# Optimization experiments

Measured on AMD Instinct MI355X. Metric: run time of the kernel, lower is better.

The kernel has to match this reference:

```python
import jax, jax.numpy as jnp
import numpy as np

# ---- Cl(4,1) geometric-product Cayley table (32 blades, metric diag(+,+,+,+,-)) ----
def _build_gp_map():
    metric = [1.0, 1.0, 1.0, 1.0, -1.0]  # e1..e4 square to +1, e5 squares to -1
    gp = np.zeros((32, 32, 32), dtype=np.float32)
    for a in range(32):          # blade a as a bitmask over 5 generators
        for b in range(32):
            # sign from reordering generators into canonical order
            swaps = 0
            t = a >> 1
            while t:
                swaps += bin(t & b).count('1')
                t >>= 1
            sign = -1.0 if (swaps & 1) else 1.0
            # sign from contracted (repeated) generators via the metric
            common = a & b
            for i in range(5):
                if common & (1 << i):
                    sign *= metric[i]
            gp[a, b, a ^ b] = sign  # e_a * e_b = sign * e_{a xor b}
    return gp

GP_MAP = _build_gp_map()  # [32, 32, 32], highly sparse (one nonzero per (a,b))
EPS = 1e-6

B, S, IN, OUT = 2, 1024, 256, 256

def setup_inputs() -> dict:
    key = jax.random.key(0)
    k1, k2 = jax.random.split(key)
    x = jax.random.normal(k1, (B, S, IN, 32), dtype=jnp.float32)
    std = 1.0 / float(np.sqrt(IN * 32))  # grade-aware Xavier scale from reset_parameters
    weight = jax.random.normal(k2, (OUT, IN, 32), dtype=jnp.float32) * std
    return {"x": x, "weight": weight}

def normalize_cl41(mv):
    # normalize each multivector by its coefficient magnitude over the 32 lanes
    norm = jnp.sqrt(jnp.sum(mv * mv, axis=-1, keepdims=True) + EPS)
    return mv / norm

def reference(x, weight):
    gp = jnp.asarray(GP_MAP, dtype=x.dtype)
    # W_op[o,i,l,k] = sum_j weight[o,i,j] * gp[j,l,k]
    W_op = jnp.einsum('oij,jlk->oilk', weight, gp)
    # out[b,s,o,k] = sum_{i,l} x[b,s,i,l] * W_op[o,i,l,k]
    out = jnp.einsum('bsil,oilk->bsok', x, W_op)
    return normalize_cl41(out)
```

## Files before the change

kernel.cpp:

```cpp
#include <hip/hip_runtime.h>
#include <hip/hip_bf16.h>
#include <stdint.h>

typedef _Float16 f16;
typedef __attribute__((ext_vector_type(8))) _Float16 f16x8;
typedef __attribute__((ext_vector_type(4))) float f32x4;

#define M_DIM 2048
#define K_FULL 8192
#define M2 8192
#define K2 2048
#define N2 2048
#define BM 256
#define BN 256
#define BK 64
#define NT (K2 / BK)
#define PSTR 260

struct CMat { int re[4][4]; int im[4][4]; };

constexpr CMat cmul(const CMat& A, const CMat& B) {
  CMat C{};
  for (int r = 0; r < 4; ++r)
    for (int c = 0; c < 4; ++c) {
      int re = 0, im = 0;
      for (int t = 0; t < 4; ++t) {
        re += A.re[r][t] * B.re[t][c] - A.im[r][t] * B.im[t][c];
        im += A.re[r][t] * B.im[t][c] + A.im[r][t] * B.re[t][c];
      }
      C.re[r][c] = re; C.im[r][c] = im;
    }
  return C;
}

constexpr int gp_sign_ct(int a, int b) {
  int sw = 0;
  for (int t = a >> 1; t; t >>= 1) {
    int x = t & b;
    while (x) { sw += x & 1; x >>= 1; }
  }
  int s = (sw & 1) ? -1 : 1;
  if ((a & b) & 16) s = -s;
  return s;
}

struct Tables {
  int8_t f_idx[32][4]; int8_t f_sgn[32][4];
  int8_t g_idx[32][4]; int8_t g_sgn[32][4];
  bool ok;
};

constexpr Tables make_tables() {
  CMat G[5] = {
    { {{0,0,0,1},{0,0,1,0},{0,1,0,0},{1,0,0,0}},
      {{0,0,0,0},{0,0,0,0},{0,0,0,0},{0,0,0,0}} },
    { {{0,0,0,0},{0,0,0,0},{0,0,0,0},{0,0,0,0}},
      {{0,0,0,-1},{0,0,1,0},{0,-1,0,0},{1,0,0,0}} },
    { {{0,0,1,0},{0,0,0,-1},{1,0,0,0},{0,-1,0,0}},
      {{0,0,0,0},{0,0,0,0},{0,0,0,0},{0,0,0,0}} },
    { {{0,0,0,0},{0,0,0,0},{0,0,0,0},{0,0,0,0}},
      {{0,0,-1,0},{0,0,0,-1},{1,0,0,0},{0,1,0,0}} },
    { {{0,0,0,0},{0,0,0,0},{0,0,0,0},{0,0,0,0}},
      {{1,0,0,0},{0,1,0,0},{0,0,-1,0},{0,0,0,-1}} } };
  CMat ID{ {{1,0,0,0},{0,1,0,0},{0,0,1,0},{0,0,0,1}},
           {{0,0,0,0},{0,0,0,0},{0,0,0,0},{0,0,0,0}} };
  CMat U[32] = {};
  for (int A = 0; A < 32; ++A) {
    CMat u = ID;
    for (int b = 0; b < 5; ++b) if (A & (1 << b)) u = cmul(u, G[b]);
    U[A] = u;
  }
  bool ok = true;
  for (int a = 0; a < 32; ++a)
    for (int b = 0; b < 32; ++b) {
      CMat P = cmul(U[a], U[b]);
      int s = gp_sign_ct(a, b);
      const CMat& T = U[a ^ b];
      for (int r = 0; r < 4; ++r)
        for (int c = 0; c < 4; ++c)
          if (P.re[r][c] != s * T.re[r][c] || P.im[r][c] != s * T.im[r][c]) ok = false;
    }
  Tables t{};
  int cnt[32] = {};
  for (int A = 0; A < 32; ++A) {
    int n = 0;
    for (int r = 0; r < 4; ++r)
      for (int c = 0; c < 4; ++c) {
        int vr = U[A].re[r][c], vi = U[A].im[r][c];
        if (vr) {
          int s = (r * 4 + c) * 2;
          if (n < 4 && cnt[s] < 4) {
            t.g_idx[A][n] = (int8_t)s; t.g_sgn[A][n] = (int8_t)vr;
            t.f_idx[s][cnt[s]] = (int8_t)A; t.f_sgn[s][cnt[s]] = (int8_t)vr;
            cnt[s]++;
          } else ok = false;
          n++;
        }
        if (vi) {
          int s = (r * 4 + c) * 2 + 1;
          if (n < 4 && cnt[s] < 4) {
            t.g_idx[A][n] = (int8_t)s; t.g_sgn[A][n] = (int8_t)vi;
            t.f_idx[s][cnt[s]] = (int8_t)A; t.f_sgn[s][cnt[s]] = (int8_t)vi;
            cnt[s]++;
          } else ok = false;
          n++;
        }
      }
    if (n != 4) ok = false;
  }
  for (int s = 0; s < 32; ++s) if (cnt[s] != 4) ok = false;
  t.ok = ok;
  return t;
}

constexpr Tables HT = make_tables();
static_assert(HT.ok, "Cl(4,1) -> M(4,C) homomorphism check FAILED");
static_assert((NT & 1) == 0, "buffer parity requires even tile count");

__device__ __forceinline__ void async16(const f16* g, f16* l) {
  __builtin_amdgcn_global_load_lds(
      (const __attribute__((address_space(1))) uint32_t*)g,
      (__attribute__((address_space(3))) uint32_t*)l,
      16, 0, 0);
}

__device__ __forceinline__ float gp_sign_rt(int a, int b) {
  int sw = 0;
  for (int t = a >> 1; t; t >>= 1) sw += __popc(t & b);
  float s = (sw & 1) ? -1.0f : 1.0f;
  if ((a & b) & 16) s = -s;
  return s;
}

#define FENCE() asm volatile("" ::: "memory")
#define BARRIER() do { FENCE(); __builtin_amdgcn_s_barrier(); FENCE(); } while (0)
#define WAIT_VM(N) asm volatile("s_waitcnt vmcnt(" #N ")" ::: "memory")

__global__ __launch_bounds__(256) void fwd_kernel(const float* __restrict__ x,
                                                  const float* __restrict__ w,
                                                  f16* __restrict__ Ag,
                                                  f16* __restrict__ Bt) {
  __shared__ float xs[256 * 33];
  const int b = blockIdx.x, t = threadIdx.x;
  const bool isx = (b < M_DIM);
  const float* src0 = isx ? (x + (size_t)b * 8192)
                          : (w + (size_t)(b - M_DIM) * 8192);
  const float4* src = (const float4*)src0;
#pragma unroll
  for (int c = t; c < 2048; c += 256) {
    float4 v = src[c];
    float* d = xs + (c >> 3) * 33 + ((c & 7) << 2);
    d[0] = v.x; d[1] = v.y; d[2] = v.z; d[3] = v.w;
  }
  __syncthreads();
  const float* xv = xs + t * 33;
  float sv[32];
#pragma unroll
  for (int s = 0; s < 32; ++s)
    sv[s] = (float)HT.f_sgn[s][0] * xv[HT.f_idx[s][0]]
          + (float)HT.f_sgn[s][1] * xv[HT.f_idx[s][1]]
          + (float)HT.f_sgn[s][2] * xv[HT.f_idx[s][2]]
          + (float)HT.f_sgn[s][3] * xv[HT.f_idx[s][3]];
  if (isx) {
#pragma unroll
    for (int c = 0; c < 4; ++c) {
      f16x8 h;
#pragma unroll
      for (int e = 0; e < 8; ++e) {
        int tt = e >> 1, p = e & 1;
        h[e] = (f16)sv[tt * 8 + c * 2 + p];
      }
      *(f16x8*)(Ag + ((size_t)(b * 4 + c)) * K2 + t * 8) = h;
    }
  } else {
    const int o = b - M_DIM;
#pragma unroll
    for (int r = 0; r < 4; ++r)
#pragma unroll
      for (int q = 0; q < 2; ++q) {
        f16x8 h;
#pragma unroll
        for (int e = 0; e < 8; ++e) {
          int tt = e >> 1, p = e & 1;
          float re = sv[(r * 4 + tt) * 2], im = sv[(r * 4 + tt) * 2 + 1];
          float v = (q == 0) ? (p == 0 ? re : -im) : (p == 0 ? im : re);
          h[e] = (f16)v;
        }
        *(f16x8*)(Bt + ((size_t)(o * 8 + r * 2 + q)) * K2 + t * 8) = h;
      }
  }
}

__global__ __launch_bounds__(512, 2) void gemm_fused_kernel(const f16* __restrict__ A,
                                                            const f16* __restrict__ Bw,
                                                            float* __restrict__ out) {
  __shared__ __align__(16) char smem[131072];
  const int t = threadIdx.x;
  const int w = t >> 6, lane = t & 63;
  const int wr = w >> 2, wc = w & 3;
  const int g = lane >> 4, lc = lane & 15;

  const int bid = blockIdx.x;
  const int swzb = (bid & 7) * 32 + (bid >> 3);
  const int by = swzb >> 3, bx = swzb & 7;
  const int m0 = by * BM, n0 = bx * BN;

  const int srow = lane >> 3;
  const int schk = (lane & 7) ^ srow;
  const f16* ga0 = A  + (size_t)(m0 + w * 8 + srow) * K2 + schk * 8;
  const f16* gb0 = Bw + (size_t)(n0 + w * 8 + srow) * K2 + schk * 8;
  const int lw = w << 10;

  const int cks0 = (g ^ (lc & 7)) << 4;
  const int cks1 = ((4 | g) ^ (lc & 7)) << 4;
  const int arow = (wr << 14) + (lc << 7);
  const int brow = 32768 + (wc << 13) + (lc << 7);

  f32x4 acc[8][4];
#pragma unroll
  for (int i = 0; i < 8; ++i)
#pragma unroll
    for (int j = 0; j < 4; ++j) {
      acc[i][j][0] = 0.f; acc[i][j][1] = 0.f; acc[i][j][2] = 0.f; acc[i][j][3] = 0.f;
    }

  f16x8 avA[4][2], avB[4][2], bvA[2][2], bvB[2][2];

#define STG_A(NBO, KK, JB) async16(ga0 + (KK) + (JB) * 131072, \
                                   (f16*)(smem + (NBO) + (JB) * 8192 + lw))
#define STG_B(NBO, KK, JB) async16(gb0 + (KK) + (JB) * 131072, \
                                   (f16*)(smem + (NBO) + 32768 + (JB) * 8192 + lw))

  STG_A(0, 0, 0); STG_A(0, 0, 1); STG_A(0, 0, 2); STG_A(0, 0, 3);
  STG_B(0, 0, 0); STG_B(0, 0, 1); STG_B(0, 0, 2); STG_B(0, 0, 3);
  WAIT_VM(0);
  BARRIER();

#pragma unroll 2
  for (int u = 0; u < NT; ++u) {
    const int bo = (u & 1) << 16;
    const int nbo = bo ^ 65536;
    const int kn = (u + 1) * BK;
    const char* ab = smem + bo + arow;
    const char* bb = smem + bo + brow;
    const bool stg = (u + 1 < NT);

#pragma unroll
    for (int i = 0; i < 4; ++i) avA[i][0] = *(const f16x8*)(ab + i * 2048 + cks0);
#pragma unroll
    for (int j = 0; j < 2; ++j) bvA[j][0] = *(const f16x8*)(bb + j * 2048 + cks0);
#pragma unroll
    for (int i = 0; i < 4; ++i) avA[i][1] = *(const f16x8*)(ab + i * 2048 + cks1);
#pragma unroll
    for (int j = 0; j < 2; ++j) bvA[j][1] = *(const f16x8*)(bb + j * 2048 + cks1);

    if (stg) {
      STG_A(nbo, kn, 0); STG_A(nbo, kn, 1); STG_A(nbo, kn, 2); STG_A(nbo, kn, 3);
      STG_B(nbo, kn, 0); STG_B(nbo, kn, 1); STG_B(nbo, kn, 2); STG_B(nbo, kn, 3);
    }

    __builtin_amdgcn_s_setprio(1);
#pragma unroll
    for (int k2 = 0; k2 < 2; ++k2)
#pragma unroll
      for (int i = 0; i < 4; ++i)
#pragma unroll
        for (int j = 0; j < 2; ++j)
          acc[i][j] = __builtin_amdgcn_mfma_f32_16x16x32_f16(avA[i][k2], bvA[j][k2],
                                                             acc[i][j], 0, 0, 0);
    __builtin_amdgcn_s_setprio(0);

#pragma unroll
    for (int j = 0; j < 2; ++j) {
      bvB[j][0] = *(const f16x8*)(bb + (2 + j) * 2048 + cks0);
      bvB[j][1] = *(const f16x8*)(bb + (2 + j) * 2048 + cks1);
    }
#pragma unroll
    for (int i = 0; i < 4; ++i) {
      avB[i][0] = *(const f16x8*)(ab + (4 + i) * 2048 + cks0);
      avB[i][1] = *(const f16x8*)(ab + (4 + i) * 2048 + cks1);
    }

    __builtin_amdgcn_s_setprio(1);
#pragma unroll
    for (int k2 = 0; k2 < 2; ++k2)
#pragma unroll
      for (int i = 0; i < 4; ++i)
#pragma unroll
        for (int j = 0; j < 2; ++j)
          acc[i][2 + j] = __builtin_amdgcn_mfma_f32_16x16x32_f16(avA[i][k2], bvB[j][k2],
                                                                 acc[i][2 + j], 0, 0, 0);
    __builtin_amdgcn_s_setprio(0);

    __builtin_amdgcn_s_setprio(1);
#pragma unroll
    for (int k2 = 0; k2 < 2; ++k2)
#pragma unroll
      for (int i = 0; i < 4; ++i)
#pragma unroll
        for (int j = 0; j < 2; ++j)
          acc[4 + i][j] = __builtin_amdgcn_mfma_f32_16x16x32_f16(avB[i][k2], bvA[j][k2],
                                                                 acc[4 + i][j], 0, 0, 0);
    __builtin_amdgcn_s_setprio(0);

    __builtin_amdgcn_s_setprio(1);
#pragma unroll
    for (int k2 = 0; k2 < 2; ++k2)
#pragma unroll
      for (int i = 0; i < 4; ++i)
#pragma unroll
        for (int j = 0; j < 2; ++j)
          acc[4 + i][2 + j] = __builtin_amdgcn_mfma_f32_16x16x32_f16(avB[i][k2], bvB[j][k2],
                                                                     acc[4 + i][2 + j], 0, 0, 0);
    __builtin_amdgcn_s_setprio(0);

    if (stg) {
      WAIT_VM(0);
      BARRIER();
    }
  }

#undef STG_B
#undef STG_A

  float* ps = (float*)smem;
  __syncthreads();
#pragma unroll
  for (int qq = 0; qq < 4; ++qq) {
    if (qq) __syncthreads();
    if (wr == (qq >> 1)) {
      const int tb = (qq & 1) << 2;
#pragma unroll
      for (int tmi = 0; tmi < 4; ++tmi) {
        const int rowl = tmi * 16 + g * 4;
#pragma unroll
        for (int tn = 0; tn < 4; ++tn) {
          const int col = wc * 64 + tn * 16 + lc;
#pragma unroll
          for (int r = 0; r < 4; ++r)
            ps[(rowl + r) * PSTR + col] = acc[tb + tmi][tn][r];
        }
      }
    }
    __syncthreads();

    const int mh = t >> 5, oh = t & 31;
    float yv[4][8];
#pragma unroll
    for (int c = 0; c < 4; ++c) {
      const float* row = ps + (mh * 4 + c) * PSTR + oh * 8;
      *(float4*)&yv[c][0] = *(const float4*)row;
      *(float4*)&yv[c][4] = *(const float4*)(row + 4);
    }
    float ss = 0.f;
#pragma unroll
    for (int c = 0; c < 4; ++c)
#pragma unroll
      for (int j = 0; j < 8; ++j) ss += yv[c][j] * yv[c][j];
    float inv = rsqrtf(0.25f * ss + 1e-6f);

    float ov[32];
#pragma unroll
    for (int k = 0; k < 32; ++k) {
      float v = 0.f;
#pragma unroll
      for (int j = 0; j < 4; ++j) {
        int s = HT.g_idx[k][j];
        int cell = s >> 1;
        int rr = cell >> 2, cc = cell & 3, pp = s & 1;
        float sgn = (float)HT.g_sgn[k][j];
        v += sgn * yv[cc][rr * 2 + pp];
      }
      ov[k] = v * 0.25f * inv;
    }
    int m = by * 64 + qq * 16 + mh;
    int o = bx * 32 + oh;
    float* op = out + (size_t)m * 8192 + o * 32;
#pragma unroll
    for (int qv = 0; qv < 8; ++qv)
      *(float4*)(op + qv * 4) = make_float4(ov[qv * 4], ov[qv * 4 + 1],
                                            ov[qv * 4 + 2], ov[qv * 4 + 3]);
  }
}

__global__ __launch_bounds__(256) void naive_vl_kernel(const float* __restrict__ x,
                                                       const float* __restrict__ w,
                                                       float* __restrict__ out) {
  __shared__ float xs[8192];
  __shared__ float sgt[1024];
  int m = blockIdx.x, o0 = blockIdx.y << 3;
  int t = threadIdx.x;
  for (int i = t; i < 1024; i += 256) {
    int kk = i >> 5, ll = i & 31;
    sgt[i] = gp_sign_rt(kk ^ ll, ll);
  }
  const float4* xr = (const float4*)(x + (size_t)m * K_FULL);
  float4* xs4 = (float4*)xs;
  for (int i = t; i < 2048; i += 256) xs4[i] = xr[i];
  __syncthreads();
  int k = t & 31, ol = t >> 5;
  int o = o0 + ol;
  const float* wrow = w + (size_t)o * K_FULL;
  float acc = 0.f;
  for (int l = 0; l < 32; ++l) {
    float s = sgt[(k << 5) + l];
    const float* wp = wrow + (k ^ l);
    const float* xp = xs + l;
    float part = 0.f;
#pragma unroll 8
    for (int i = 0; i < 256; ++i) part += xp[i << 5] * wp[i << 5];
    acc += part * s;
  }
  float ss = acc * acc;
  for (int msk = 1; msk < 32; msk <<= 1) ss += __shfl_xor(ss, msk, 32);
  out[((size_t)m * 256 + o) * 32 + k] = acc * rsqrtf(ss + 1e-6f);
}

extern "C" void kernel_launch(void* const* d_in, const int* in_sizes, int n_in,
                              void* d_out, int out_size, void* d_ws, size_t ws_size,
                              hipStream_t stream) {
  const float* x = (const float*)d_in[0];
  const float* w = (const float*)d_in[1];
  float* out = (float*)d_out;

  size_t agE = (size_t)M2 * K2;
  size_t btE = (size_t)N2 * K2;
  size_t need = (agE + btE) * sizeof(f16);

  if (ws_size >= need) {
    f16* Ag = (f16*)d_ws;
    f16* Bt = Ag + agE;
    fwd_kernel<<<dim3(M_DIM + 256), dim3(256), 0, stream>>>(x, w, Ag, Bt);
    gemm_fused_kernel<<<dim3((M2 / BM) * (N2 / BN)), dim3(512), 0, stream>>>(Ag, Bt, out);
  } else {
    naive_vl_kernel<<<dim3(M_DIM, 32), dim3(256), 0, stream>>>(x, w, out);
  }
}
```

Baseline: 191.3 us.

## Use 1024-thread GEMM blocks with smaller per-wave tiles; load fwd inputs via registers

The GEMM kernel moves from 512 to 1024 threads per block. Each of the 16 waves now computes a 64x64 output tile with a 4x4 accumulator array instead of 128x64, and global-to-LDS staging is spread over more waves. The aim is more latency hiding through extra waves, at the cost of lower per-wave reuse, the loss of the 2-blocks-per-CU hint, and an epilogue that only uses half the threads. The preprocessing kernel also drops its shared-memory transpose and has each thread read its own 32 floats straight into registers.

Result: slower. 209.7 us (+9.6%).

```diff
diff --git a/kernel.cpp b/kernel.cpp
--- a/kernel.cpp
+++ b/kernel.cpp
@@ -140,27 +140,22 @@
                                                   const float* __restrict__ w,
                                                   f16* __restrict__ Ag,
                                                   f16* __restrict__ Bt) {
-  __shared__ float xs[256 * 33];
   const int b = blockIdx.x, t = threadIdx.x;
   const bool isx = (b < M_DIM);
-  const float* src0 = isx ? (x + (size_t)b * 8192)
-                          : (w + (size_t)(b - M_DIM) * 8192);
-  const float4* src = (const float4*)src0;
-#pragma unroll
-  for (int c = t; c < 2048; c += 256) {
-    float4 v = src[c];
-    float* d = xs + (c >> 3) * 33 + ((c & 7) << 2);
-    d[0] = v.x; d[1] = v.y; d[2] = v.z; d[3] = v.w;
-  }
-  __syncthreads();
-  const float* xv = xs + t * 33;
+  const float* src = isx ? (x + ((size_t)b * 256 + t) * 32)
+                         : (w + ((size_t)(b - M_DIM) * 256 + t) * 32);
+  float xr[32];
+#pragma unroll
+  for (int q = 0; q < 8; ++q)
+    *(float4*)&xr[q * 4] = *(const float4*)(src + q * 4);
+
   float sv[32];
 #pragma unroll
   for (int s = 0; s < 32; ++s)
-    sv[s] = (float)HT.f_sgn[s][0] * xv[HT.f_idx[s][0]]
-          + (float)HT.f_sgn[s][1] * xv[HT.f_idx[s][1]]
-          + (float)HT.f_sgn[s][2] * xv[HT.f_idx[s][2]]
-          + (float)HT.f_sgn[s][3] * xv[HT.f_idx[s][3]];
+    sv[s] = (float)HT.f_sgn[s][0] * xr[HT.f_idx[s][0]]
+          + (float)HT.f_sgn[s][1] * xr[HT.f_idx[s][1]]
+          + (float)HT.f_sgn[s][2] * xr[HT.f_idx[s][2]]
+          + (float)HT.f_sgn[s][3] * xr[HT.f_idx[s][3]];
   if (isx) {
 #pragma unroll
     for (int c = 0; c < 4; ++c) {
@@ -191,9 +186,9 @@
   }
 }
 
-__global__ __launch_bounds__(512, 2) void gemm_fused_kernel(const f16* __restrict__ A,
-                                                            const f16* __restrict__ Bw,
-                                                            float* __restrict__ out) {
+__global__ __launch_bounds__(1024) void gemm_fused_kernel(const f16* __restrict__ A,
+                                                          const f16* __restrict__ Bw,
+                                                          float* __restrict__ out) {
   __shared__ __align__(16) char smem[131072];
   const int t = threadIdx.x;
   const int w = t >> 6, lane = t & 63;
@@ -213,30 +208,26 @@
 
   const int cks0 = (g ^ (lc & 7)) << 4;
   const int cks1 = ((4 | g) ^ (lc & 7)) << 4;
-  const int arow = (wr << 14) + (lc << 7);
+  const int arow = (wr << 13) + (lc << 7);
   const int brow = 32768 + (wc << 13) + (lc << 7);
 
-  f32x4 acc[8][4];
-#pragma unroll
-  for (int i = 0; i < 8; ++i)
+  f32x4 acc[4][4];
+#pragma unroll
+  for (int i = 0; i < 4; ++i)
 #pragma unroll
     for (int j = 0; j < 4; ++j) {
       acc[i][j][0] = 0.f; acc[i][j][1] = 0.f; acc[i][j][2] = 0.f; acc[i][j][3] = 0.f;
     }
 
-  f16x8 avA[4][2], avB[4][2], bvA[2][2], bvB[2][2];
-
-#define STG_A(NBO, KK, JB) async16(ga0 + (KK) + (JB) * 131072, \
-                                   (f16*)(smem + (NBO) + (JB) * 8192 + lw))
-#define STG_B(NBO, KK, JB) async16(gb0 + (KK) + (JB) * 131072, \
-                                   (f16*)(smem + (NBO) + 32768 + (JB) * 8192 + lw))
-
-  STG_A(0, 0, 0); STG_A(0, 0, 1); STG_A(0, 0, 2); STG_A(0, 0, 3);
-  STG_B(0, 0, 0); STG_B(0, 0, 1); STG_B(0, 0, 2); STG_B(0, 0, 3);
+#define STG_A(NBO, KK, JB) async16(ga0 + (KK) + (JB) * 262144, \
+                                   (f16*)(smem + (NBO) + (JB) * 16384 + lw))
+#define STG_B(NBO, KK, JB) async16(gb0 + (KK) + (JB) * 262144, \
+                                   (f16*)(smem + (NBO) + 32768 + (JB) * 16384 + lw))
+
+  STG_A(0, 0, 0); STG_A(0, 0, 1); STG_B(0, 0, 0); STG_B(0, 0, 1);
   WAIT_VM(0);
   BARRIER();
 
-#pragma unroll 2
   for (int u = 0; u < NT; ++u) {
     const int bo = (u & 1) << 16;
     const int nbo = bo ^ 65536;
@@ -245,73 +236,34 @@
     const char* bb = smem + bo + brow;
     const bool stg = (u + 1 < NT);
 
-#pragma unroll
-    for (int i = 0; i < 4; ++i) avA[i][0] = *(const f16x8*)(ab + i * 2048 + cks0);
-#pragma unroll
-    for (int j = 0; j < 2; ++j) bvA[j][0] = *(const f16x8*)(bb + j * 2048 + cks0);
-#pragma unroll
-    for (int i = 0; i < 4; ++i) avA[i][1] = *(const f16x8*)(ab + i * 2048 + cks1);
-#pragma unroll
-    for (int j = 0; j < 2; ++j) bvA[j][1] = *(const f16x8*)(bb + j * 2048 + cks1);
-
-    if (stg) {
-      STG_A(nbo, kn, 0); STG_A(nbo, kn, 1); STG_A(nbo, kn, 2); STG_A(nbo, kn, 3);
-      STG_B(nbo, kn, 0); STG_B(nbo, kn, 1); STG_B(nbo, kn, 2); STG_B(nbo, kn, 3);
-    }
-
+    if (stg) { STG_A(nbo, kn, 0); STG_A(nbo, kn, 1);
+               STG_B(nbo, kn, 0); STG_B(nbo, kn, 1); }
+
+    f16x8 av[4], bv[4];
+#pragma unroll
+    for (int i = 0; i < 4; ++i) av[i] = *(const f16x8*)(ab + (i << 11) + cks0);
+#pragma unroll
+    for (int j = 0; j < 4; ++j) bv[j] = *(const f16x8*)(bb + (j << 11) + cks0);
     __builtin_amdgcn_s_setprio(1);
 #pragma unroll
-    for (int k2 = 0; k2 < 2; ++k2)
-#pragma unroll
-      for (int i = 0; i < 4; ++i)
-#pragma unroll
-        for (int j = 0; j < 2; ++j)
-          acc[i][j] = __builtin_amdgcn_mfma_f32_16x16x32_f16(avA[i][k2], bvA[j][k2],
-                                                             acc[i][j], 0, 0, 0);
+    for (int i = 0; i < 4; ++i)
+#pragma unroll
+      for (int j = 0; j < 4; ++j)
+        acc[i][j] = __builtin_amdgcn_mfma_f32_16x16x32_f16(av[i], bv[j],
+                                                           acc[i][j], 0, 0, 0);
     __builtin_amdgcn_s_setprio(0);
-
-#pragma unroll
-    for (int j = 0; j < 2; ++j) {
-      bvB[j][0] = *(const f16x8*)(bb + (2 + j) * 2048 + cks0);
-      bvB[j][1] = *(const f16x8*)(bb + (2 + j) * 2048 + cks1);
-    }
-#pragma unroll
-    for (int i = 0; i < 4; ++i) {
-      avB[i][0] = *(const f16x8*)(ab + (4 + i) * 2048 + cks0);
-      avB[i][1] = *(const f16x8*)(ab + (4 + i) * 2048 + cks1);
-    }
-
+    FENCE();
+#pragma unroll
+    for (int i = 0; i < 4; ++i) av[i] = *(const f16x8*)(ab + (i << 11) + cks1);
+#pragma unroll
+    for (int j = 0; j < 4; ++j) bv[j] = *(const f16x8*)(bb + (j << 11) + cks1);
     __builtin_amdgcn_s_setprio(1);
 #pragma unroll
-    for (int k2 = 0; k2 < 2; ++k2)
-#pragma unroll
-      for (int i = 0; i < 4; ++i)
-#pragma unroll
-        for (int j = 0; j < 2; ++j)
-          acc[i][2 + j] = __builtin_amdgcn_mfma_f32_16x16x32_f16(avA[i][k2], bvB[j][k2],
-                                                                 acc[i][2 + j], 0, 0, 0);
-    __builtin_amdgcn_s_setprio(0);
-
-    __builtin_amdgcn_s_setprio(1);
-#pragma unroll
-    for (int k2 = 0; k2 < 2; ++k2)
-#pragma unroll
-      for (int i = 0; i < 4; ++i)
-#pragma unroll
-        for (int j = 0; j < 2; ++j)
-          acc[4 + i][j] = __builtin_amdgcn_mfma_f32_16x16x32_f16(avB[i][k2], bvA[j][k2],
-                                                                 acc[4 + i][j], 0, 0, 0);
-    __builtin_amdgcn_s_setprio(0);
-
-    __builtin_amdgcn_s_setprio(1);
-#pragma unroll
-    for (int k2 = 0; k2 < 2; ++k2)
-#pragma unroll
-      for (int i = 0; i < 4; ++i)
-#pragma unroll
-        for (int j = 0; j < 2; ++j)
-          acc[4 + i][2 + j] = __builtin_amdgcn_mfma_f32_16x16x32_f16(avB[i][k2], bvB[j][k2],
-                                                                     acc[4 + i][2 + j], 0, 0, 0);
+    for (int i = 0; i < 4; ++i)
+#pragma unroll
+      for (int j = 0; j < 4; ++j)
+        acc[i][j] = __builtin_amdgcn_mfma_f32_16x16x32_f16(av[i], bv[j],
+                                                           acc[i][j], 0, 0, 0);
     __builtin_amdgcn_s_setprio(0);
 
     if (stg) {
@@ -328,58 +280,60 @@
 #pragma unroll
   for (int qq = 0; qq < 4; ++qq) {
     if (qq) __syncthreads();
-    if (wr == (qq >> 1)) {
-      const int tb = (qq & 1) << 2;
-#pragma unroll
-      for (int tmi = 0; tmi < 4; ++tmi) {
-        const int rowl = tmi * 16 + g * 4;
-#pragma unroll
-        for (int tn = 0; tn < 4; ++tn) {
-          const int col = wc * 64 + tn * 16 + lc;
+    if (wr == qq) {
+#pragma unroll
+      for (int i = 0; i < 4; ++i) {
+        const int rowl = i * 16 + g * 4;
+#pragma unroll
+        for (int j = 0; j < 4; ++j) {
+          const int col = wc * 64 + j * 16 + lc;
 #pragma unroll
           for (int r = 0; r < 4; ++r)
-            ps[(rowl + r) * PSTR + col] = acc[tb + tmi][tn][r];
+            ps[(rowl + r) * PSTR + col] = acc[i][j][r];
         }
       }
     }
     __syncthreads();
 
-    const int mh = t >> 5, oh = t & 31;
-    float yv[4][8];
-#pragma unroll
-    for (int c = 0; c < 4; ++c) {
-      const float* row = ps + (mh * 4 + c) * PSTR + oh * 8;
-      *(float4*)&yv[c][0] = *(const float4*)row;
-      *(float4*)&yv[c][4] = *(const float4*)(row + 4);
-    }
-    float ss = 0.f;
-#pragma unroll
-    for (int c = 0; c < 4; ++c)
-#pragma unroll
-      for (int j = 0; j < 8; ++j) ss += yv[c][j] * yv[c][j];
-    float inv = rsqrtf(0.25f * ss + 1e-6f);
-
-    float ov[32];
-#pragma unroll
-    for (int k = 0; k < 32; ++k) {
-      float v = 0.f;
-#pragma unroll
-      for (int j = 0; j < 4; ++j) {
-        int s = HT.g_idx[k][j];
-        int cell = s >> 1;
-        int rr = cell >> 2, cc = cell & 3, pp = s & 1;
-        float sgn = (float)HT.g_sgn[k][j];
-        v += sgn * yv[cc][rr * 2 + pp];
-      }
-      ov[k] = v * 0.25f * inv;
-    }
-    int m = by * 64 + qq * 16 + mh;
-    int o = bx * 32 + oh;
-    float* op = out + (size_t)m * 8192 + o * 32;
-#pragma unroll
-    for (int qv = 0; qv < 8; ++qv)
-      *(float4*)(op + qv * 4) = make_float4(ov[qv * 4], ov[qv * 4 + 1],
-                                            ov[qv * 4 + 2], ov[qv * 4 + 3]);
+    if (t < 512) {
+      const int mh = t >> 5, oh = t & 31;
+      float yv[4][8];
+#pragma unroll
+      for (int c = 0; c < 4; ++c) {
+        const float* row = ps + (mh * 4 + c) * PSTR + oh * 8;
+        *(float4*)&yv[c][0] = *(const float4*)row;
+        *(float4*)&yv[c][4] = *(const float4*)(row + 4);
+      }
+      float ss = 0.f;
+#pragma unroll
+      for (int c = 0; c < 4; ++c)
+#pragma unroll
+        for (int j = 0; j < 8; ++j) ss += yv[c][j] * yv[c][j];
+      float inv = rsqrtf(0.25f * ss + 1e-6f);
+      const float sc = 0.25f * inv;
+
+      int m = by * 64 + qq * 16 + mh;
+      int o = bx * 32 + oh;
+      float* op = out + (size_t)m * 8192 + o * 32;
+#pragma unroll
+      for (int q = 0; q < 8; ++q) {
+        float ovq[4];
+#pragma unroll
+        for (int d = 0; d < 4; ++d) {
+          const int k = q * 4 + d;
+          float v = 0.f;
+#pragma unroll
+          for (int j = 0; j < 4; ++j) {
+            int s = HT.g_idx[k][j];
+            int cell = s >> 1;
+            int rr = cell >> 2, cc = cell & 3, pp = s & 1;
+            v += (float)HT.g_sgn[k][j] * yv[cc][rr * 2 + pp];
+          }
+          ovq[d] = v * sc;
+        }
+        *(float4*)(op + q * 4) = make_float4(ovq[0], ovq[1], ovq[2], ovq[3]);
+      }
+    }
   }
 }
 
@@ -431,7 +385,7 @@
     f16* Ag = (f16*)d_ws;
     f16* Bt = Ag + agE;
     fwd_kernel<<<dim3(M_DIM + 256), dim3(256), 0, stream>>>(x, w, Ag, Bt);
-    gemm_fused_kernel<<<dim3((M2 / BM) * (N2 / BN)), dim3(512), 0, stream>>>(Ag, Bt, out);
+    gemm_fused_kernel<<<dim3((M2 / BM) * (N2 / BN)), dim3(1024), 0, stream>>>(Ag, Bt, out);
   } else {
     naive_vl_kernel<<<dim3(M_DIM, 32), dim3(256), 0, stream>>>(x, w, out);
   }
```

## Load B fragments directly from global into registers, stage only A in LDS

Applied to the files above, without the earlier changes.

Operand B is no longer staged through shared memory. Each wave reads its B fragments straight from global memory into registers every K step, and only A stays double-buffered in LDS. This halves the LDS footprint, which could allow higher occupancy, and removes the LDS traffic for B. The cost is uncoalesced, latency-exposed global loads on the critical path, extra barriers inside the loop, and removal of the unroll-2 pragma.

Result: slower. 238.5 us (+24.7%).

```diff
diff --git a/kernel.cpp b/kernel.cpp
--- a/kernel.cpp
+++ b/kernel.cpp
@@ -194,7 +194,7 @@
 __global__ __launch_bounds__(512, 2) void gemm_fused_kernel(const f16* __restrict__ A,
                                                             const f16* __restrict__ Bw,
                                                             float* __restrict__ out) {
-  __shared__ __align__(16) char smem[131072];
+  __shared__ __align__(16) char smem[66560];
   const int t = threadIdx.x;
   const int w = t >> 6, lane = t & 63;
   const int wr = w >> 2, wc = w & 3;
@@ -207,14 +207,14 @@
 
   const int srow = lane >> 3;
   const int schk = (lane & 7) ^ srow;
-  const f16* ga0 = A  + (size_t)(m0 + w * 8 + srow) * K2 + schk * 8;
-  const f16* gb0 = Bw + (size_t)(n0 + w * 8 + srow) * K2 + schk * 8;
+  const f16* ga0 = A + (size_t)(m0 + w * 8 + srow) * K2 + schk * 8;
   const int lw = w << 10;
 
   const int cks0 = (g ^ (lc & 7)) << 4;
   const int cks1 = ((4 | g) ^ (lc & 7)) << 4;
   const int arow = (wr << 14) + (lc << 7);
-  const int brow = 32768 + (wc << 13) + (lc << 7);
+
+  const f16* gbf = Bw + (size_t)(n0 + (wc << 6) + lc) * K2 + (g << 3);
 
   f32x4 acc[8][4];
 #pragma unroll
@@ -224,103 +224,68 @@
       acc[i][j][0] = 0.f; acc[i][j][1] = 0.f; acc[i][j][2] = 0.f; acc[i][j][3] = 0.f;
     }
 
-  f16x8 avA[4][2], avB[4][2], bvA[2][2], bvB[2][2];
-
 #define STG_A(NBO, KK, JB) async16(ga0 + (KK) + (JB) * 131072, \
                                    (f16*)(smem + (NBO) + (JB) * 8192 + lw))
-#define STG_B(NBO, KK, JB) async16(gb0 + (KK) + (JB) * 131072, \
-                                   (f16*)(smem + (NBO) + 32768 + (JB) * 8192 + lw))
 
   STG_A(0, 0, 0); STG_A(0, 0, 1); STG_A(0, 0, 2); STG_A(0, 0, 3);
-  STG_B(0, 0, 0); STG_B(0, 0, 1); STG_B(0, 0, 2); STG_B(0, 0, 3);
   WAIT_VM(0);
   BARRIER();
 
-#pragma unroll 2
   for (int u = 0; u < NT; ++u) {
-    const int bo = (u & 1) << 16;
-    const int nbo = bo ^ 65536;
+    const int bo = (u & 1) << 15;
+    const int nbo = bo ^ 32768;
     const int kn = (u + 1) * BK;
     const char* ab = smem + bo + arow;
-    const char* bb = smem + bo + brow;
     const bool stg = (u + 1 < NT);
 
-#pragma unroll
-    for (int i = 0; i < 4; ++i) avA[i][0] = *(const f16x8*)(ab + i * 2048 + cks0);
-#pragma unroll
-    for (int j = 0; j < 2; ++j) bvA[j][0] = *(const f16x8*)(bb + j * 2048 + cks0);
-#pragma unroll
-    for (int i = 0; i < 4; ++i) avA[i][1] = *(const f16x8*)(ab + i * 2048 + cks1);
-#pragma unroll
-    for (int j = 0; j < 2; ++j) bvA[j][1] = *(const f16x8*)(bb + j * 2048 + cks1);
-
-    if (stg) {
-      STG_A(nbo, kn, 0); STG_A(nbo, kn, 1); STG_A(nbo, kn, 2); STG_A(nbo, kn, 3);
-      STG_B(nbo, kn, 0); STG_B(nbo, kn, 1); STG_B(nbo, kn, 2); STG_B(nbo, kn, 3);
-    }
-
+    f16x8 av[4][2], bv[4][2];
+#pragma unroll
+    for (int j = 0; j < 4; ++j) {
+      bv[j][0] = *(const f16x8*)(gbf + (size_t)j * 32768 + u * 64);
+      bv[j][1] = *(const f16x8*)(gbf + (size_t)j * 32768 + u * 64 + 32);
+    }
+    FENCE();
+    if (stg) { STG_A(nbo, kn, 0); STG_A(nbo, kn, 1);
+               STG_A(nbo, kn, 2); STG_A(nbo, kn, 3); }
+
+#pragma unroll
+    for (int i = 0; i < 4; ++i) {
+      av[i][0] = *(const f16x8*)(ab + i * 2048 + cks0);
+      av[i][1] = *(const f16x8*)(ab + i * 2048 + cks1);
+    }
+    BARRIER();
     __builtin_amdgcn_s_setprio(1);
 #pragma unroll
     for (int k2 = 0; k2 < 2; ++k2)
 #pragma unroll
       for (int i = 0; i < 4; ++i)
 #pragma unroll
-        for (int j = 0; j < 2; ++j)
-          acc[i][j] = __builtin_amdgcn_mfma_f32_16x16x32_f16(avA[i][k2], bvA[j][k2],
+        for (int j = 0; j < 4; ++j)
+          acc[i][j] = __builtin_amdgcn_mfma_f32_16x16x32_f16(av[i][k2], bv[j][k2],
                                                              acc[i][j], 0, 0, 0);
     __builtin_amdgcn_s_setprio(0);
-
-#pragma unroll
-    for (int j = 0; j < 2; ++j) {
-      bvB[j][0] = *(const f16x8*)(bb + (2 + j) * 2048 + cks0);
-      bvB[j][1] = *(const f16x8*)(bb + (2 + j) * 2048 + cks1);
-    }
+    BARRIER();
+
 #pragma unroll
     for (int i = 0; i < 4; ++i) {
-      avB[i][0] = *(const f16x8*)(ab + (4 + i) * 2048 + cks0);
-      avB[i][1] = *(const f16x8*)(ab + (4 + i) * 2048 + cks1);
-    }
-
+      av[i][0] = *(const f16x8*)(ab + (4 + i) * 2048 + cks0);
+      av[i][1] = *(const f16x8*)(ab + (4 + i) * 2048 + cks1);
+    }
+    BARRIER();
     __builtin_amdgcn_s_setprio(1);
 #pragma unroll
     for (int k2 = 0; k2 < 2; ++k2)
 #pragma unroll
       for (int i = 0; i < 4; ++i)
 #pragma unroll
-        for (int j = 0; j < 2; ++j)
-          acc[i][2 + j] = __builtin_amdgcn_mfma_f32_16x16x32_f16(avA[i][k2], bvB[j][k2],
-                                                                 acc[i][2 + j], 0, 0, 0);
-    __builtin_amdgcn_s_setprio(0);
-
-    __builtin_amdgcn_s_setprio(1);
-#pragma unroll
-    for (int k2 = 0; k2 < 2; ++k2)
-#pragma unroll
-      for (int i = 0; i < 4; ++i)
-#pragma unroll
-        for (int j = 0; j < 2; ++j)
-          acc[4 + i][j] = __builtin_amdgcn_mfma_f32_16x16x32_f16(avB[i][k2], bvA[j][k2],
+        for (int j = 0; j < 4; ++j)
+          acc[4 + i][j] = __builtin_amdgcn_mfma_f32_16x16x32_f16(av[i][k2], bv[j][k2],
                                                                  acc[4 + i][j], 0, 0, 0);
     __builtin_amdgcn_s_setprio(0);
-
-    __builtin_amdgcn_s_setprio(1);
-#pragma unroll
-    for (int k2 = 0; k2 < 2; ++k2)
-#pragma unroll
-      for (int i = 0; i < 4; ++i)
-#pragma unroll
-        for (int j = 0; j < 2; ++j)
-          acc[4 + i][2 + j] = __builtin_amdgcn_mfma_f32_16x16x32_f16(avB[i][k2], bvB[j][k2],
-                                                                     acc[4 + i][2 + j], 0, 0, 0);
-    __builtin_amdgcn_s_setprio(0);
-
-    if (stg) {
-      WAIT_VM(0);
-      BARRIER();
-    }
-  }
-
-#undef STG_B
+    if (stg) WAIT_VM(0);
+    BARRIER();
+  }
+
 #undef STG_A
 
   float* ps = (float*)smem;
```
